# Optimization experiments

Measured on AMD Instinct MI355X. Metric: run time of the kernel, lower is better.

Reference implementation:

```python
import jax, jax.numpy as jnp
import numpy as np

D_STATE = 16
D_CONV = 4


def rmsnorm(x, w, eps=1e-6):
    # normalize over last (channel) axis
    return x * jax.lax.rsqrt(jnp.mean(x * x, axis=-1, keepdims=True) + eps) * w


def silu(x):
    return x * jax.nn.sigmoid(x)


def mamba(x, in_proj_w, conv1d_w, conv1d_b, x_proj_w, dt_proj_w, dt_proj_b, A_log, D_param, out_proj_w):
    # x: [B, L, C], d_inner == C (expand=1)
    B, L, C = x.shape
    dt_rank = dt_proj_w.shape[1]
    xz = jnp.einsum('blc,ec->ble', x, in_proj_w)  # [B, L, 2C]
    u, z = jnp.split(xz, 2, axis=-1)
    # causal depthwise conv1d over time (pad left d_conv-1)
    uc = jax.lax.conv_general_dilated(
        u.transpose(0, 2, 1), conv1d_w[:, None, :], (1,), [(D_CONV - 1, 0)],
        dimension_numbers=('NCH', 'OIH', 'NCH'), feature_group_count=C)
    u = silu((uc + conv1d_b[None, :, None]).transpose(0, 2, 1))  # [B, L, C]
    x_dbl = jnp.einsum('blc,ec->ble', u, x_proj_w)  # [B, L, dt_rank + 2*N]
    dt, Bm, Cm = jnp.split(x_dbl, [dt_rank, dt_rank + D_STATE], axis=-1)
    delta = jax.nn.softplus(jnp.einsum('blr,dr->bld', dt, dt_proj_w) + dt_proj_b)  # [B, L, C]
    A = -jnp.exp(A_log)  # [C, N]
    deltaA = jnp.exp(delta[..., None] * A)              # [B, L, C, N]
    deltaBu = (delta * u)[..., None] * Bm[:, :, None, :]  # [B, L, C, N]

    def step(h, inp):
        dA, dBu, c = inp
        h = dA * h + dBu
        return h, jnp.einsum('bdn,bn->bd', h, c)

    h0 = jnp.zeros((B, C, D_STATE), x.dtype)
    _, ys = jax.lax.scan(step, h0, (deltaA.transpose(1, 0, 2, 3),
                                    deltaBu.transpose(1, 0, 2, 3),
                                    Cm.transpose(1, 0, 2)))
    y = ys.transpose(1, 0, 2) + u * D_param  # [B, L, C]
    y = y * silu(z)
    return jnp.einsum('bld,od->blo', y, out_proj_w)


def reference(x, norm_w, in_proj_w, conv1d_w, conv1d_b, x_proj_w, dt_proj_w, dt_proj_b,
              A_log, D_param, out_proj_w, scale_mod, dw_w, dw_b, res_scale):
    B, C, H, W = x.shape
    x_cl = x.transpose(0, 2, 3, 1)              # [B, H, W, C]
    xn_cl = rmsnorm(x_cl, norm_w)
    x_norm = xn_cl.transpose(0, 3, 1, 2)        # [B, C, H, W]
    # bidirectional Mamba over flattened spatial sequence
    x_flat = xn_cl.reshape(B, H * W, C)
    mparams = (in_proj_w, conv1d_w, conv1d_b, x_proj_w, dt_proj_w, dt_proj_b, A_log, D_param, out_proj_w)
    fwd = mamba(x_flat, *mparams)
    bwd = jnp.flip(mamba(jnp.flip(x_flat, axis=1), *mparams), axis=1)
    g = (fwd + bwd) * scale_mod
    global_feat = g.reshape(B, H, W, C).transpose(0, 3, 1, 2)
    # local spatial gating: sigmoid(depthwise 3x3 conv) * x_norm
    conv = jax.lax.conv_general_dilated(
        x_norm, dw_w[:, None, :, :], (1, 1), [(1, 1), (1, 1)],
        dimension_numbers=('NCHW', 'OIHW', 'NCHW'), feature_group_count=C)
    local_feat = jax.nn.sigmoid(conv + dw_b[None, :, None, None]) * x_norm
    return x + res_scale * (global_feat + local_feat)


def setup_inputs() -> dict:
    key = jax.random.key(0)
    ks = jax.random.split(key, 10)
    B, C, H, W = 8, 384, 32, 32
    dt_rank = 24  # ceil(384 / 16)
    s = 0.02
    f32 = jnp.float32
    return {
        'x': jax.random.normal(ks[0], (B, C, H, W), f32),
        'norm_w': jnp.ones((C,), f32),
        'in_proj_w': jax.random.normal(ks[1], (2 * C, C), f32) * s,
        'conv1d_w': jax.random.normal(ks[2], (C, D_CONV), f32) * 0.2,
        'conv1d_b': jnp.zeros((C,), f32),
        'x_proj_w': jax.random.normal(ks[3], (dt_rank + 2 * D_STATE, C), f32) * s,
        'dt_proj_w': jax.random.normal(ks[4], (C, dt_rank), f32) * 0.1,
        'dt_proj_b': jax.random.uniform(ks[5], (C,), f32, -4.0, -2.0),
        'A_log': jnp.log(jnp.tile(jnp.arange(1, D_STATE + 1, dtype=f32), (C, 1))),
        'D_param': jnp.ones((C,), f32),
        'out_proj_w': jax.random.normal(ks[6], (C, C), f32) * s,
        'scale_mod': jnp.full((1,), 0.25, f32),
        'dw_w': jax.random.normal(ks[7], (C, 3, 3), f32) * 0.1,
        'dw_b': jnp.zeros((C,), f32),
        'res_scale': jnp.full((1,), 0.5, f32),
    }
```

## Files before the change

kernel.cpp:

```cpp
#include <hip/hip_runtime.h>
#include <hip/hip_bf16.h>


typedef __attribute__((ext_vector_type(8))) short bf16x8;
typedef __attribute__((ext_vector_type(8))) unsigned short u16x8;
typedef __attribute__((ext_vector_type(4))) float f32x4;

#define L2E 1.44269504088896340736f

static __device__ __forceinline__ unsigned short f2bf(float f) {
  unsigned int u = __builtin_bit_cast(unsigned int, f);
  u += 0x7fff + ((u >> 16) & 1);
  return (unsigned short)(u >> 16);
}
static __device__ __forceinline__ float bf2f(unsigned short u) {
  unsigned int v = (unsigned int)u << 16;
  return __builtin_bit_cast(float, v);
}

#define GLOAD_LDS16(g, l)                                             \
  __builtin_amdgcn_global_load_lds(                                   \
      (const __attribute__((address_space(1))) unsigned int*)(g),     \
      (__attribute__((address_space(3))) unsigned int*)(l), 16, 0, 0)

__global__ __launch_bounds__(256) void prep_k(
    const float* __restrict__ in_w, const float* __restrict__ x_w,
    const float* __restrict__ dt_w, const float* __restrict__ out_w,
    const float* __restrict__ A_log, const float* __restrict__ nw,
    unsigned short* __restrict__ W_in, unsigned short* __restrict__ W_x,
    unsigned short* __restrict__ W_dt, unsigned short* __restrict__ W_out,
    float* __restrict__ A2) {
  int idx = blockIdx.x * 256 + threadIdx.x;
  switch (blockIdx.y) {
    case 0: if (idx < 768 * 384) W_in[idx] = f2bf(in_w[idx] * nw[idx % 384]); break;
    case 1: if (idx < 64 * 384) { int n = idx / 384, k = idx - n * 384;
              W_x[idx] = f2bf(n < 56 ? x_w[n * 384 + k] : 0.f); } break;
    case 2: if (idx < 384 * 32) { int n = idx >> 5, k = idx & 31;
              W_dt[idx] = f2bf(k < 24 ? dt_w[n * 24 + k] : 0.f); } break;
    case 3: if (idx < 384 * 384) W_out[idx] = f2bf(out_w[idx]); break;
    case 4: if (idx < 384 * 16) A2[idx] = -expf(A_log[idx]) * L2E; break;
  }
}

__global__ __launch_bounds__(256) void transpose_k(
    const float* __restrict__ x, unsigned short* __restrict__ xb,
    float* __restrict__ nf) {
  const int b = blockIdx.y;
  const int l0 = blockIdx.x * 32;
  const int tid = threadIdx.x;
  const int cr = tid >> 5, lw = tid & 31;
  const int cj = tid & 63, lr = tid >> 6;
  __shared__ float t64[64][33];
  __shared__ float part[8][33];
  float acc = 0.f;
  for (int cc = 0; cc < 6; ++cc) {
    #pragma unroll
    for (int k = 0; k < 8; ++k) {
      int cp = k * 8 + cr;
      int c = cc * 64 + cp;
      float v = x[(((size_t)(b * 384 + c)) << 10) + l0 + lw];
      t64[cp][lw] = v;
      acc = fmaf(v, v, acc);
    }
    __syncthreads();
    #pragma unroll
    for (int k2 = 0; k2 < 8; ++k2) {
      int ll = lr + 4 * k2;
      xb[((size_t)((b << 10) + l0 + ll)) * 384 + cc * 64 + cj] = f2bf(t64[cj][ll]);
    }
    __syncthreads();
  }
  part[cr][lw] = acc;
  __syncthreads();
  if (tid < 32) {
    float s = part[0][tid] + part[1][tid] + part[2][tid] + part[3][tid] +
              part[4][tid] + part[5][tid] + part[6][tid] + part[7][tid];
    nf[(b << 10) + l0 + tid] = rsqrtf(s * (1.f / 384.f) + 1e-6f);
  }
}

template <int EPI, int SUMIN>
__global__ __launch_bounds__(256) void gemm128_k(
    const unsigned short* __restrict__ A0u, const unsigned short* __restrict__ A1u,
    const unsigned short* __restrict__ Bw, int K, int N,
    float* __restrict__ outf, unsigned short* __restrict__ outb,
    const float* __restrict__ aux) {
  __shared__ __attribute__((aligned(16))) unsigned short As[128 * 32];
  __shared__ __attribute__((aligned(16))) unsigned short Bs[128 * 32];
  const int n0 = blockIdx.x * 128, m0 = blockIdx.y * 128;
  const int tid = threadIdx.x;
  const int lane = tid & 63, wave = tid >> 6;
  const int wm = wave >> 1, wn = wave & 1;
  const int fr = lane & 15, ks = (lane >> 4) * 8;
  const int row = tid >> 2, colseg = (tid & 3) * 8;
  const unsigned short* pA0 = A0u + (size_t)(m0 + row) * K + colseg;
  const unsigned short* pA1 = A0u + (size_t)(m0 + 64 + row) * K + colseg;
  const unsigned short* pB0 = Bw + (size_t)(n0 + row) * K + colseg;
  const unsigned short* pB1 = Bw + (size_t)(n0 + 64 + row) * K + colseg;
  unsigned short* lA0 = As + wave * 512;
  unsigned short* lA1 = As + 2048 + wave * 512;
  unsigned short* lB0 = Bs + wave * 512;
  unsigned short* lB1 = Bs + 2048 + wave * 512;
  f32x4 acc[4][4] = {};
  for (int k0 = 0; k0 < K; k0 += 32) {
    __syncthreads();
    if (SUMIN) {
      #pragma unroll
      for (int p = 0; p < 2; ++p) {
        int r = p * 64 + row;
        u16x8 va = *(const u16x8*)&A0u[(size_t)(m0 + r) * K + k0 + colseg];
        u16x8 vb = *(const u16x8*)&A1u[(size_t)(m0 + r) * K + k0 + colseg];
        u16x8 s;
        #pragma unroll
        for (int j = 0; j < 8; ++j) s[j] = f2bf(bf2f(va[j]) + bf2f(vb[j]));
        *(u16x8*)&As[r * 32 + colseg] = s;
      }
    } else {
      GLOAD_LDS16(pA0, lA0);
      GLOAD_LDS16(pA1, lA1);
      pA0 += 32; pA1 += 32;
    }
    GLOAD_LDS16(pB0, lB0);
    GLOAD_LDS16(pB1, lB1);
    pB0 += 32; pB1 += 32;
    __syncthreads();
    bf16x8 af[4], bf[4];
    #pragma unroll
    for (int mi = 0; mi < 4; ++mi)
      af[mi] = *(const bf16x8*)&As[(wm * 64 + mi * 16 + fr) * 32 + ks];
    #pragma unroll
    for (int ni = 0; ni < 4; ++ni)
      bf[ni] = *(const bf16x8*)&Bs[(wn * 64 + ni * 16 + fr) * 32 + ks];
    #pragma unroll
    for (int mi = 0; mi < 4; ++mi)
      #pragma unroll
      for (int ni = 0; ni < 4; ++ni)
        acc[mi][ni] = __builtin_amdgcn_mfma_f32_16x16x32_bf16(af[mi], bf[ni], acc[mi][ni], 0, 0, 0);
  }
  #pragma unroll
  for (int mi = 0; mi < 4; ++mi)
    #pragma unroll
    for (int ni = 0; ni < 4; ++ni)
      #pragma unroll
      for (int j = 0; j < 4; ++j) {
        int m = m0 + wm * 64 + mi * 16 + (lane >> 4) * 4 + j;
        int n = n0 + wn * 64 + ni * 16 + fr;
        float v = acc[mi][ni][j];
        if (EPI == 0) {
          outb[(size_t)m * N + n] = f2bf(v * aux[m]);
        } else {
          outf[(size_t)m * N + n] = v * aux[0];
        }
      }
}

template <int EPI>
__global__ __launch_bounds__(256) void gemm_k(
    const unsigned short* __restrict__ A0u, const unsigned short* __restrict__ A1u,
    const unsigned short* __restrict__ Bw, int K, int N,
    float* __restrict__ of0, float* __restrict__ of1,
    unsigned short* __restrict__ ob0, unsigned short* __restrict__ ob1,
    const float* __restrict__ aux) {
  const unsigned short* A = blockIdx.z ? A1u : A0u;
  float* outf = blockIdx.z ? of1 : of0;
  unsigned short* outb = blockIdx.z ? ob1 : ob0;
  __shared__ unsigned short As[64][40];
  __shared__ unsigned short Bs[64][40];
  const int n0 = blockIdx.x * 64, m0 = blockIdx.y * 64;
  const int tid = threadIdx.x;
  const int lane = tid & 63, wave = tid >> 6;
  const int wm = wave >> 1, wn = wave & 1;
  const int lrow = tid >> 2, lseg = (tid & 3) * 8;
  const int fr = lane & 15, ks = (lane >> 4) * 8;
  f32x4 acc[2][2] = {};
  for (int k0 = 0; k0 < K; k0 += 32) {
    __syncthreads();
    *(bf16x8*)&As[lrow][lseg] = *(const bf16x8*)&A[(size_t)(m0 + lrow) * K + k0 + lseg];
    *(bf16x8*)&Bs[lrow][lseg] = *(const bf16x8*)&Bw[(size_t)(n0 + lrow) * K + k0 + lseg];
    __syncthreads();
    bf16x8 a0 = *(const bf16x8*)&As[wm * 32 + fr][ks];
    bf16x8 a1 = *(const bf16x8*)&As[wm * 32 + 16 + fr][ks];
    bf16x8 b0 = *(const bf16x8*)&Bs[wn * 32 + fr][ks];
    bf16x8 b1 = *(const bf16x8*)&Bs[wn * 32 + 16 + fr][ks];
    acc[0][0] = __builtin_amdgcn_mfma_f32_16x16x32_bf16(a0, b0, acc[0][0], 0, 0, 0);
    acc[0][1] = __builtin_amdgcn_mfma_f32_16x16x32_bf16(a0, b1, acc[0][1], 0, 0, 0);
    acc[1][0] = __builtin_amdgcn_mfma_f32_16x16x32_bf16(a1, b0, acc[1][0], 0, 0, 0);
    acc[1][1] = __builtin_amdgcn_mfma_f32_16x16x32_bf16(a1, b1, acc[1][1], 0, 0, 0);
  }
  #pragma unroll
  for (int mi = 0; mi < 2; ++mi)
    #pragma unroll
    for (int ni = 0; ni < 2; ++ni)
      #pragma unroll
      for (int j = 0; j < 4; ++j) {
        int m = m0 + wm * 32 + mi * 16 + (lane >> 4) * 4 + j;
        int n = n0 + wn * 32 + ni * 16 + (lane & 15);
        float v = acc[mi][ni][j];
        if (EPI == 1) {
          if (n < 24) outb[m * 32 + n] = f2bf(v);
          else if (n < 32) outb[m * 32 + n] = 0;
          if (n >= 24 && n < 56) outf[m * 32 + (n - 24)] = v;
        } else {
          float t = v + aux[n];
          float sp = (t > 20.f) ? t : log1pf(expf(t));
          outb[(size_t)m * N + n] = f2bf(sp);
        }
      }
}

__global__ __launch_bounds__(384) void conv_silu_k(
    const unsigned short* __restrict__ xz, const float* __restrict__ cw,
    const float* __restrict__ cb,
    unsigned short* __restrict__ ub0, unsigned short* __restrict__ ub1) {
  const int st = blockIdx.x, b = blockIdx.y, dir = blockIdx.z;
  const int c = threadIdx.x;
  const int s0 = st * 8;
  const float w0 = cw[c * 4 + 0], w1 = cw[c * 4 + 1];
  const float w2 = cw[c * 4 + 2], w3 = cw[c * 4 + 3];
  const float bb = cb[c];
  unsigned short* ub = dir ? ub1 : ub0;
  float xv[11];
  #pragma unroll
  for (int k = 0; k < 11; ++k) {
    int j = s0 - 3 + k;
    float v = 0.f;
    if (j >= 0) {
      int t = dir ? (1023 - j) : j;
      v = bf2f(xz[(size_t)((b << 10) + t) * 768 + c]);
    }
    xv[k] = v;
  }
  #pragma unroll
  for (int s = 0; s < 8; ++s) {
    float a = bb + xv[s] * w0 + xv[s + 1] * w1 + xv[s + 2] * w2 + xv[s + 3] * w3;
    float uv = a * __builtin_amdgcn_rcpf(1.f + __builtin_amdgcn_exp2f(-a * L2E));
    ub[(size_t)((b << 10) + s0 + s) * 384 + c] = f2bf(uv);
  }
}

__global__ __launch_bounds__(512) void scan1_k(
    const unsigned short* __restrict__ de0, const unsigned short* __restrict__ de1,
    const unsigned short* __restrict__ ub0, const unsigned short* __restrict__ ub1,
    const float* __restrict__ bc0, const float* __restrict__ bc1,
    const float* __restrict__ A2, float* __restrict__ PH) {
  const int ct = blockIdx.x, b = blockIdx.y;
  const int dir = blockIdx.z >> 4, seg = blockIdx.z & 15;
  const unsigned short* del = dir ? de1 : de0;
  const unsigned short* uu  = dir ? ub1 : ub0;
  const float* bc  = dir ? bc1 : bc0;
  const int tid = threadIdx.x;
  const int lane = tid & 63, wave = tid >> 6;
  const int n = lane & 15, cg = lane >> 4;
  const int cl = wave * 4 + cg;
  const int c = ct * 32 + cl;
  const float a2 = A2[c * 16 + n];
  const size_t base = ((size_t)b << 10) + seg * 64;
  __shared__ __attribute__((aligned(16))) float sd[32][68];
  __shared__ __attribute__((aligned(16))) float su[32][68];
  __shared__ __attribute__((aligned(16))) float sB[16][68];
  const int li = tid >> 5, lj = tid & 31;
  const int li3 = tid >> 4, lj3 = tid & 15;
  unsigned short rd[4], ru[4];
  float rb[2];
  #pragma unroll
  for (int k = 0; k < 4; ++k) {
    size_t rowi = base + k * 16 + li;
    rd[k] = del[rowi * 384 + ct * 32 + lj];
    ru[k] = uu [rowi * 384 + ct * 32 + lj];
  }
  #pragma unroll
  for (int k = 0; k < 2; ++k)
    rb[k] = bc[(base + k * 32 + li3) * 32 + lj3];
  #pragma unroll
  for (int k = 0; k < 4; ++k) {
    sd[lj][k * 16 + li] = bf2f(rd[k]);
    su[lj][k * 16 + li] = bf2f(ru[k]);
  }
  #pragma unroll
  for (int k = 0; k < 2; ++k) sB[lj3][k * 32 + li3] = rb[k];
  __syncthreads();
  float h = 0.f, P = 1.f;
  for (int ch = 0; ch < 4; ++ch) {
    f32x4 dv[4], uv4[4], bmv[4];
    #pragma unroll
    for (int r = 0; r < 4; ++r) {
      dv[r]  = *(const f32x4*)&sd[cl][ch * 16 + r * 4];
      uv4[r] = *(const f32x4*)&su[cl][ch * 16 + r * 4];
      bmv[r] = *(const f32x4*)&sB[n][ch * 16 + r * 4];
    }
    #pragma unroll
    for (int i = 0; i < 16; ++i) {
      float dd = dv[i >> 2][i & 3];
      float dA = __builtin_amdgcn_exp2f(dd * a2);
      h = fmaf(dA, h, dd * uv4[i >> 2][i & 3] * bmv[i >> 2][i & 3]);
      P *= dA;
    }
  }
  size_t o = (size_t)((dir * 8 + b) * 16 + seg) * 6144 + c * 16 + n;
  *(float2*)&PH[o * 2] = make_float2(P, h);
}

__global__ __launch_bounds__(512) void scan2_k(
    const unsigned short* __restrict__ de0, const unsigned short* __restrict__ de1,
    const unsigned short* __restrict__ ub0, const unsigned short* __restrict__ ub1,
    const float* __restrict__ bc0, const float* __restrict__ bc1,
    const unsigned short* __restrict__ xz, const float* __restrict__ A2,
    const float* __restrict__ Dp, const float* __restrict__ PH,
    unsigned short* __restrict__ Sb0, unsigned short* __restrict__ Sb1) {
  const int ct = blockIdx.x, b = blockIdx.y;
  const int dir = blockIdx.z >> 4, seg = blockIdx.z & 15;
  const unsigned short* del = dir ? de1 : de0;
  const unsigned short* uu  = dir ? ub1 : ub0;
  const float* bc  = dir ? bc1 : bc0;
  unsigned short* S = dir ? Sb1 : Sb0;
  const int tid = threadIdx.x;
  const int lane = tid & 63, wave = tid >> 6;
  const int n = lane & 15, cg = lane >> 4;
  const int cl = wave * 4 + cg;
  const int c = ct * 32 + cl;
  const float a2 = A2[c * 16 + n];
  const float dpc = Dp[c];
  const size_t base = (size_t)b << 10;
  const int segoff = seg * 64;
  __shared__ __attribute__((aligned(16))) float sd[32][68];
  __shared__ __attribute__((aligned(16))) float su[32][68];
  __shared__ __attribute__((aligned(16))) float sz[32][68];
  __shared__ __attribute__((aligned(16))) float sbc[32][68];
  const int li = tid >> 5, lj = tid & 31;
  unsigned short rd[4], ru[4], rz[4];
  float rb[4];
  #pragma unroll
  for (int k = 0; k < 4; ++k) {
    size_t rowi = base + segoff + k * 16 + li;
    rd[k] = del[rowi * 384 + ct * 32 + lj];
    ru[k] = uu [rowi * 384 + ct * 32 + lj];
    int t = dir ? (1023 - (segoff + k * 16 + li)) : (segoff + k * 16 + li);
    rz[k] = xz[(base + t) * 768 + 384 + ct * 32 + lj];
    rb[k] = bc[rowi * 32 + lj];
  }
  float h = 0.f;
  {
    size_t rb2 = ((size_t)((dir * 8 + b) * 16) * 6144 + c * 16 + n) * 2;
    #pragma unroll
    for (int s = 0; s < 15; ++s) {
      float2 ph = *(const float2*)&PH[rb2 + (size_t)s * 12288];
      h = (s < seg) ? fmaf(ph.x, h, ph.y) : h;
    }
  }
  #pragma unroll
  for (int k = 0; k < 4; ++k) {
    sd[lj][k * 16 + li] = bf2f(rd[k]);
    su[lj][k * 16 + li] = bf2f(ru[k]);
    sz[lj][k * 16 + li] = bf2f(rz[k]);
    sbc[lj][k * 16 + li] = rb[k];
  }
  __syncthreads();
  for (int ch = 0; ch < 4; ++ch) {
    f32x4 dv[4], uv4[4], bmv[4], cmv[4];
    #pragma unroll
    for (int r = 0; r < 4; ++r) {
      dv[r]  = *(const f32x4*)&sd[cl][ch * 16 + r * 4];
      uv4[r] = *(const f32x4*)&su[cl][ch * 16 + r * 4];
      bmv[r] = *(const f32x4*)&sbc[n][ch * 16 + r * 4];
      cmv[r] = *(const f32x4*)&sbc[16 + n][ch * 16 + r * 4];
    }
    float p[16];
    #pragma unroll
    for (int i = 0; i < 16; ++i) {
      float dd = dv[i >> 2][i & 3];
      float dA = __builtin_amdgcn_exp2f(dd * a2);
      h = fmaf(dA, h, dd * uv4[i >> 2][i & 3] * bmv[i >> 2][i & 3]);
      p[i] = h * cmv[i >> 2][i & 3];
    }
    float q8[8];
    #pragma unroll
    for (int j = 0; j < 8; ++j) {
      float send = (n & 8) ? p[j] : p[j + 8];
      float recv = __shfl_xor(send, 8);
      float keep = (n & 8) ? p[j + 8] : p[j];
      q8[j] = keep + recv;
    }
    float q4[4];
    #pragma unroll
    for (int j = 0; j < 4; ++j) {
      float send = (n & 4) ? q8[j] : q8[j + 4];
      float recv = __shfl_xor(send, 4);
      float keep = (n & 4) ? q8[j + 4] : q8[j];
      q4[j] = keep + recv;
    }
    float q2[2];
    #pragma unroll
    for (int j = 0; j < 2; ++j) {
      float send = (n & 2) ? q4[j] : q4[j + 2];
      float recv = __shfl_xor(send, 2);
      float keep = (n & 2) ? q4[j + 2] : q4[j];
      q2[j] = keep + recv;
    }
    float send = (n & 1) ? q2[0] : q2[1];
    float recv = __shfl_xor(send, 1);
    float keep = (n & 1) ? q2[1] : q2[0];
    float ysum = keep + recv;
    float uvn = su[cl][ch * 16 + n];
    float zz  = sz[cl][ch * 16 + n];
    float sig = __builtin_amdgcn_rcpf(1.f + __builtin_amdgcn_exp2f(-zz * L2E));
    float y = (ysum + uvn * dpc) * (zz * sig);
    int s = segoff + ch * 16 + n;
    int t = dir ? (1023 - s) : s;
    S[(base + t) * 384 + c] = f2bf(y);
  }
}

__global__ __launch_bounds__(256) void final_k(
    const float* __restrict__ G, const unsigned short* __restrict__ xb,
    const float* __restrict__ nf, const float* __restrict__ nw,
    const float* __restrict__ x, const float* __restrict__ dww,
    const float* __restrict__ dwb, const float* __restrict__ rs,
    float* __restrict__ out) {
  __shared__ float tile[64][33];
  __shared__ float wq[9][64];
  __shared__ float bbs[64], nws[64];
  const int l0 = blockIdx.x * 32, c0 = blockIdx.y * 64, b = blockIdx.z;
  const int tid = threadIdx.x;
  for (int i = tid; i < 576; i += 256) {
    int c = i / 9, q = i - c * 9;
    wq[q][c] = dww[(size_t)(c0 + c) * 9 + q] * nw[c0 + c];
  }
  if (tid < 64) { bbs[tid] = dwb[c0 + tid]; nws[tid] = nw[c0 + tid]; }
  __syncthreads();
  {
    const int oct = tid & 7, li = tid >> 3;
    const int l = l0 + li;
    const int hh = l >> 5, ww = l & 31;
    float acc[8];
    {
      f32x4 ba = *(const f32x4*)&bbs[oct * 8];
      f32x4 bb2 = *(const f32x4*)&bbs[oct * 8 + 4];
      #pragma unroll
      for (int j = 0; j < 4; ++j) { acc[j] = ba[j]; acc[j + 4] = bb2[j]; }
    }
    #pragma unroll
    for (int di = -1; di <= 1; ++di) {
      int h2 = hh + di;
      if (h2 < 0 || h2 > 31) continue;
      #pragma unroll
      for (int dj = -1; dj <= 1; ++dj) {
        int w2 = ww + dj;
        if (w2 < 0 || w2 > 31) continue;
        int lp = h2 * 32 + w2;
        float nfl = nf[(b << 10) + lp];
        u16x8 v = *(const u16x8*)&xb[(size_t)((b << 10) + lp) * 384 + c0 + oct * 8];
        int q = (di + 1) * 3 + (dj + 1);
        f32x4 wa = *(const f32x4*)&wq[q][oct * 8];
        f32x4 wb = *(const f32x4*)&wq[q][oct * 8 + 4];
        #pragma unroll
        for (int j = 0; j < 4; ++j) {
          acc[j]     = fmaf(bf2f(v[j]) * nfl, wa[j], acc[j]);
          acc[j + 4] = fmaf(bf2f(v[j + 4]) * nfl, wb[j], acc[j + 4]);
        }
      }
    }
    size_t ri = (size_t)((b << 10) + l) * 384 + c0 + oct * 8;
    float nfl0 = nf[(b << 10) + l];
    u16x8 xc = *(const u16x8*)&xb[ri];
    f32x4 g0 = *(const f32x4*)&G[ri];
    f32x4 g1 = *(const f32x4*)&G[ri + 4];
    #pragma unroll
    for (int j = 0; j < 8; ++j) {
      float xv = bf2f(xc[j]) * nfl0 * nws[oct * 8 + j];
      float sig = __builtin_amdgcn_rcpf(1.f + __builtin_amdgcn_exp2f(-acc[j] * L2E));
      float gg = (j < 4) ? g0[j] : g1[j - 4];
      tile[oct * 8 + j][li] = gg + xv * sig;
    }
  }
  __syncthreads();
  {
    const int lw = tid & 31, cr = tid >> 5;
    const float rsv = rs[0];
    for (int p = 0; p < 8; ++p) {
      int c = c0 + p * 8 + cr;
      size_t o = ((size_t)(b * 384 + c) << 10) + l0 + lw;
      out[o] = x[o] + rsv * tile[p * 8 + cr][lw];
    }
  }
}

extern "C" void kernel_launch(void* const* d_in, const int* in_sizes, int n_in,
                              void* d_out, int out_size, void* d_ws, size_t ws_size,
                              hipStream_t stream) {
  const float* x         = (const float*)d_in[0];
  const float* norm_w    = (const float*)d_in[1];
  const float* in_proj_w = (const float*)d_in[2];
  const float* conv1d_w  = (const float*)d_in[3];
  const float* conv1d_b  = (const float*)d_in[4];
  const float* x_proj_w  = (const float*)d_in[5];
  const float* dt_proj_w = (const float*)d_in[6];
  const float* dt_proj_b = (const float*)d_in[7];
  const float* A_log     = (const float*)d_in[8];
  const float* D_param   = (const float*)d_in[9];
  const float* out_proj_w= (const float*)d_in[10];
  const float* scale_mod = (const float*)d_in[11];
  const float* dw_w      = (const float*)d_in[12];
  const float* dw_b      = (const float*)d_in[13];
  const float* res_scale = (const float*)d_in[14];
  float* out = (float*)d_out;

  char* base = (char*)d_ws;
  size_t off = 0;
  auto alloc = [&](size_t bytes) {
    off = (off + 255) & ~(size_t)255;
    void* p = base + off;
    off += bytes;
    return p;
  };
  const size_t B_BLC = (size_t)8192 * 384 * 2;

  unsigned short* xb   = (unsigned short*)alloc(B_BLC);
  float*          nf   = (float*)alloc((size_t)8192 * 4);
  unsigned short* xz   = (unsigned short*)alloc((size_t)8192 * 768 * 2);
  unsigned short* u_b0 = (unsigned short*)alloc(B_BLC);
  unsigned short* u_b1 = (unsigned short*)alloc(B_BLC);
  unsigned short* dtp0 = (unsigned short*)alloc((size_t)8192 * 32 * 2);
  unsigned short* dtp1 = (unsigned short*)alloc((size_t)8192 * 32 * 2);
  float*          bc0  = (float*)alloc((size_t)8192 * 32 * 4);
  float*          bc1  = (float*)alloc((size_t)8192 * 32 * 4);
  unsigned short* de0  = (unsigned short*)alloc(B_BLC);
  unsigned short* de1  = (unsigned short*)alloc(B_BLC);
  unsigned short* Sb0  = (unsigned short*)alloc(B_BLC);
  unsigned short* Sb1  = (unsigned short*)alloc(B_BLC);
  float*          PH   = (float*)alloc((size_t)1572864 * 2 * 4);
  unsigned short* W_in = (unsigned short*)alloc((size_t)768 * 384 * 2);
  unsigned short* W_x  = (unsigned short*)alloc((size_t)64 * 384 * 2);
  unsigned short* W_dt = (unsigned short*)alloc((size_t)384 * 32 * 2);
  unsigned short* W_out= (unsigned short*)alloc((size_t)384 * 384 * 2);
  float*          A2   = (float*)alloc((size_t)384 * 16 * 4);
  float*          G    = (float*)alloc((size_t)8192 * 384 * 4);

  prep_k<<<dim3(1152, 5), 256, 0, stream>>>(in_proj_w, x_proj_w, dt_proj_w,
                                            out_proj_w, A_log, norm_w,
                                            W_in, W_x, W_dt, W_out, A2);
  transpose_k<<<dim3(32, 8), 256, 0, stream>>>(x, xb, nf);
  gemm128_k<0, 0><<<dim3(6, 64), 256, 0, stream>>>(xb, xb, W_in, 384, 768,
                                                   nullptr, xz, nf);
  conv_silu_k<<<dim3(128, 8, 2), 384, 0, stream>>>(xz, conv1d_w, conv1d_b,
                                                   u_b0, u_b1);
  gemm_k<1><<<dim3(1, 128, 2), 256, 0, stream>>>(u_b0, u_b1, W_x, 384, 64,
                                                 bc0, bc1, dtp0, dtp1, nullptr);
  gemm_k<2><<<dim3(6, 128, 2), 256, 0, stream>>>(dtp0, dtp1, W_dt, 32, 384,
                                                 nullptr, nullptr, de0, de1,
                                                 dt_proj_b);
  scan1_k<<<dim3(12, 8, 32), 512, 0, stream>>>(de0, de1, u_b0, u_b1, bc0, bc1,
                                               A2, PH);
  scan2_k<<<dim3(12, 8, 32), 512, 0, stream>>>(de0, de1, u_b0, u_b1, bc0, bc1,
                                               xz, A2, D_param, PH, Sb0, Sb1);
  gemm128_k<3, 1><<<dim3(3, 64), 256, 0, stream>>>(Sb0, Sb1, W_out, 384, 384,
                                                   G, nullptr, scale_mod);
  final_k<<<dim3(32, 6, 8), 256, 0, stream>>>(G, xb, nf, norm_w, x, dw_w, dw_b,
                                              res_scale, out);
}
```

Baseline: 247.3 us.

## Fold dt_proj into x_proj weights, store out-proj result in bf16, stage scan output

Precomputes a combined weight dt_proj_w·x_proj_w[:24], so delta and the B/C projections come from one 128-tiled GEMM with a softplus epilogue. This replaces two small GEMM launches and the dt intermediate buffer. The out-proj GEMM now writes bf16 instead of fp32 to halve that intermediate's traffic, at some precision cost. scan1 precomputes delta*u when staging, and scan2 stages its outputs in LDS so global stores are coalesced. The combined GEMM does more arithmetic (K=384 over N=512 instead of rank 24).

```diff
diff --git a/kernel.cpp b/kernel.cpp
--- a/kernel.cpp
+++ b/kernel.cpp
@@ -27,18 +27,24 @@
     const float* __restrict__ in_w, const float* __restrict__ x_w,
     const float* __restrict__ dt_w, const float* __restrict__ out_w,
     const float* __restrict__ A_log, const float* __restrict__ nw,
-    unsigned short* __restrict__ W_in, unsigned short* __restrict__ W_x,
-    unsigned short* __restrict__ W_dt, unsigned short* __restrict__ W_out,
-    float* __restrict__ A2) {
+    unsigned short* __restrict__ W_in, unsigned short* __restrict__ W_out,
+    unsigned short* __restrict__ Wcomb, float* __restrict__ A2) {
   int idx = blockIdx.x * 256 + threadIdx.x;
   switch (blockIdx.y) {
     case 0: if (idx < 768 * 384) W_in[idx] = f2bf(in_w[idx] * nw[idx % 384]); break;
-    case 1: if (idx < 64 * 384) { int n = idx / 384, k = idx - n * 384;
-              W_x[idx] = f2bf(n < 56 ? x_w[n * 384 + k] : 0.f); } break;
-    case 2: if (idx < 384 * 32) { int n = idx >> 5, k = idx & 31;
-              W_dt[idx] = f2bf(k < 24 ? dt_w[n * 24 + k] : 0.f); } break;
-    case 3: if (idx < 384 * 384) W_out[idx] = f2bf(out_w[idx]); break;
-    case 4: if (idx < 384 * 16) A2[idx] = -expf(A_log[idx]) * L2E; break;
+    case 1: if (idx < 384 * 384) W_out[idx] = f2bf(out_w[idx]); break;
+    case 2: if (idx < 384 * 16) A2[idx] = -expf(A_log[idx]) * L2E; break;
+    case 3: if (idx < 384 * 384) {
+        int o = idx / 384, c = idx - o * 384;
+        float s = 0.f;
+        #pragma unroll
+        for (int r = 0; r < 24; ++r) s += dt_w[o * 24 + r] * x_w[r * 384 + c];
+        Wcomb[idx] = f2bf(s);
+      } break;
+    case 4: if (idx < 128 * 384) {
+        int n = idx / 384, k = idx - n * 384;
+        Wcomb[147456 + idx] = f2bf(n < 32 ? x_w[(24 + n) * 384 + k] : 0.f);
+      } break;
   }
 }
 
@@ -83,8 +89,12 @@
 __global__ __launch_bounds__(256) void gemm128_k(
     const unsigned short* __restrict__ A0u, const unsigned short* __restrict__ A1u,
     const unsigned short* __restrict__ Bw, int K, int N,
-    float* __restrict__ outf, unsigned short* __restrict__ outb,
+    unsigned short* __restrict__ ob0, unsigned short* __restrict__ ob1,
+    float* __restrict__ of0, float* __restrict__ of1,
     const float* __restrict__ aux) {
+  const unsigned short* Au = (EPI == 2 && blockIdx.z) ? A1u : A0u;
+  unsigned short* ob = (EPI == 2 && blockIdx.z) ? ob1 : ob0;
+  float* of = (EPI == 2 && blockIdx.z) ? of1 : of0;
   __shared__ __attribute__((aligned(16))) unsigned short As[128 * 32];
   __shared__ __attribute__((aligned(16))) unsigned short Bs[128 * 32];
   const int n0 = blockIdx.x * 128, m0 = blockIdx.y * 128;
@@ -93,8 +103,8 @@
   const int wm = wave >> 1, wn = wave & 1;
   const int fr = lane & 15, ks = (lane >> 4) * 8;
   const int row = tid >> 2, colseg = (tid & 3) * 8;
-  const unsigned short* pA0 = A0u + (size_t)(m0 + row) * K + colseg;
-  const unsigned short* pA1 = A0u + (size_t)(m0 + 64 + row) * K + colseg;
+  const unsigned short* pA0 = Au + (size_t)(m0 + row) * K + colseg;
+  const unsigned short* pA1 = Au + (size_t)(m0 + 64 + row) * K + colseg;
   const unsigned short* pB0 = Bw + (size_t)(n0 + row) * K + colseg;
   const unsigned short* pB1 = Bw + (size_t)(n0 + 64 + row) * K + colseg;
   unsigned short* lA0 = As + wave * 512;
@@ -124,18 +134,18 @@
     GLOAD_LDS16(pB1, lB1);
     pB0 += 32; pB1 += 32;
     __syncthreads();
-    bf16x8 af[4], bf[4];
+    bf16x8 af[4], bfr[4];
     #pragma unroll
     for (int mi = 0; mi < 4; ++mi)
       af[mi] = *(const bf16x8*)&As[(wm * 64 + mi * 16 + fr) * 32 + ks];
     #pragma unroll
     for (int ni = 0; ni < 4; ++ni)
-      bf[ni] = *(const bf16x8*)&Bs[(wn * 64 + ni * 16 + fr) * 32 + ks];
+      bfr[ni] = *(const bf16x8*)&Bs[(wn * 64 + ni * 16 + fr) * 32 + ks];
     #pragma unroll
     for (int mi = 0; mi < 4; ++mi)
       #pragma unroll
       for (int ni = 0; ni < 4; ++ni)
-        acc[mi][ni] = __builtin_amdgcn_mfma_f32_16x16x32_bf16(af[mi], bf[ni], acc[mi][ni], 0, 0, 0);
+        acc[mi][ni] = __builtin_amdgcn_mfma_f32_16x16x32_bf16(af[mi], bfr[ni], acc[mi][ni], 0, 0, 0);
   }
   #pragma unroll
   for (int mi = 0; mi < 4; ++mi)
@@ -147,63 +157,17 @@
         int n = n0 + wn * 64 + ni * 16 + fr;
         float v = acc[mi][ni][j];
         if (EPI == 0) {
-          outb[(size_t)m * N + n] = f2bf(v * aux[m]);
+          ob0[(size_t)m * N + n] = f2bf(v * aux[m]);
+        } else if (EPI == 2) {
+          if (n < 384) {
+            float t = v + aux[n];
+            float sp = (t > 20.f) ? t : log1pf(expf(t));
+            ob[(size_t)m * 384 + n] = f2bf(sp);
+          } else if (n < 416) {
+            of[(size_t)m * 32 + (n - 384)] = v;
+          }
         } else {
-          outf[(size_t)m * N + n] = v * aux[0];
-        }
-      }
-}
-
-template <int EPI>
-__global__ __launch_bounds__(256) void gemm_k(
-    const unsigned short* __restrict__ A0u, const unsigned short* __restrict__ A1u,
-    const unsigned short* __restrict__ Bw, int K, int N,
-    float* __restrict__ of0, float* __restrict__ of1,
-    unsigned short* __restrict__ ob0, unsigned short* __restrict__ ob1,
-    const float* __restrict__ aux) {
-  const unsigned short* A = blockIdx.z ? A1u : A0u;
-  float* outf = blockIdx.z ? of1 : of0;
-  unsigned short* outb = blockIdx.z ? ob1 : ob0;
-  __shared__ unsigned short As[64][40];
-  __shared__ unsigned short Bs[64][40];
-  const int n0 = blockIdx.x * 64, m0 = blockIdx.y * 64;
-  const int tid = threadIdx.x;
-  const int lane = tid & 63, wave = tid >> 6;
-  const int wm = wave >> 1, wn = wave & 1;
-  const int lrow = tid >> 2, lseg = (tid & 3) * 8;
-  const int fr = lane & 15, ks = (lane >> 4) * 8;
-  f32x4 acc[2][2] = {};
-  for (int k0 = 0; k0 < K; k0 += 32) {
-    __syncthreads();
-    *(bf16x8*)&As[lrow][lseg] = *(const bf16x8*)&A[(size_t)(m0 + lrow) * K + k0 + lseg];
-    *(bf16x8*)&Bs[lrow][lseg] = *(const bf16x8*)&Bw[(size_t)(n0 + lrow) * K + k0 + lseg];
-    __syncthreads();
-    bf16x8 a0 = *(const bf16x8*)&As[wm * 32 + fr][ks];
-    bf16x8 a1 = *(const bf16x8*)&As[wm * 32 + 16 + fr][ks];
-    bf16x8 b0 = *(const bf16x8*)&Bs[wn * 32 + fr][ks];
-    bf16x8 b1 = *(const bf16x8*)&Bs[wn * 32 + 16 + fr][ks];
-    acc[0][0] = __builtin_amdgcn_mfma_f32_16x16x32_bf16(a0, b0, acc[0][0], 0, 0, 0);
-    acc[0][1] = __builtin_amdgcn_mfma_f32_16x16x32_bf16(a0, b1, acc[0][1], 0, 0, 0);
-    acc[1][0] = __builtin_amdgcn_mfma_f32_16x16x32_bf16(a1, b0, acc[1][0], 0, 0, 0);
-    acc[1][1] = __builtin_amdgcn_mfma_f32_16x16x32_bf16(a1, b1, acc[1][1], 0, 0, 0);
-  }
-  #pragma unroll
-  for (int mi = 0; mi < 2; ++mi)
-    #pragma unroll
-    for (int ni = 0; ni < 2; ++ni)
-      #pragma unroll
-      for (int j = 0; j < 4; ++j) {
-        int m = m0 + wm * 32 + mi * 16 + (lane >> 4) * 4 + j;
-        int n = n0 + wn * 32 + ni * 16 + (lane & 15);
-        float v = acc[mi][ni][j];
-        if (EPI == 1) {
-          if (n < 24) outb[m * 32 + n] = f2bf(v);
-          else if (n < 32) outb[m * 32 + n] = 0;
-          if (n >= 24 && n < 56) outf[m * 32 + (n - 24)] = v;
-        } else {
-          float t = v + aux[n];
-          float sp = (t > 20.f) ? t : log1pf(expf(t));
-          outb[(size_t)m * N + n] = f2bf(sp);
+          ob0[(size_t)m * N + n] = f2bf(v * aux[0]);
         }
       }
 }
@@ -273,26 +237,26 @@
     rb[k] = bc[(base + k * 32 + li3) * 32 + lj3];
   #pragma unroll
   for (int k = 0; k < 4; ++k) {
-    sd[lj][k * 16 + li] = bf2f(rd[k]);
-    su[lj][k * 16 + li] = bf2f(ru[k]);
+    float dd = bf2f(rd[k]);
+    sd[lj][k * 16 + li] = dd;
+    su[lj][k * 16 + li] = dd * bf2f(ru[k]);
   }
   #pragma unroll
   for (int k = 0; k < 2; ++k) sB[lj3][k * 32 + li3] = rb[k];
   __syncthreads();
   float h = 0.f, P = 1.f;
   for (int ch = 0; ch < 4; ++ch) {
-    f32x4 dv[4], uv4[4], bmv[4];
+    f32x4 dv[4], duv[4], bmv[4];
     #pragma unroll
     for (int r = 0; r < 4; ++r) {
       dv[r]  = *(const f32x4*)&sd[cl][ch * 16 + r * 4];
-      uv4[r] = *(const f32x4*)&su[cl][ch * 16 + r * 4];
+      duv[r] = *(const f32x4*)&su[cl][ch * 16 + r * 4];
       bmv[r] = *(const f32x4*)&sB[n][ch * 16 + r * 4];
     }
     #pragma unroll
     for (int i = 0; i < 16; ++i) {
-      float dd = dv[i >> 2][i & 3];
-      float dA = __builtin_amdgcn_exp2f(dd * a2);
-      h = fmaf(dA, h, dd * uv4[i >> 2][i & 3] * bmv[i >> 2][i & 3]);
+      float dA = __builtin_amdgcn_exp2f(dv[i >> 2][i & 3] * a2);
+      h = fmaf(dA, h, duv[i >> 2][i & 3] * bmv[i >> 2][i & 3]);
       P *= dA;
     }
   }
@@ -320,27 +284,28 @@
   const int c = ct * 32 + cl;
   const float a2 = A2[c * 16 + n];
   const float dpc = Dp[c];
-  const size_t base = (size_t)b << 10;
+  const size_t bb_ = (size_t)b << 10;
   const int segoff = seg * 64;
   __shared__ __attribute__((aligned(16))) float sd[32][68];
   __shared__ __attribute__((aligned(16))) float su[32][68];
   __shared__ __attribute__((aligned(16))) float sz[32][68];
   __shared__ __attribute__((aligned(16))) float sbc[32][68];
+  __shared__ __attribute__((aligned(16))) unsigned short sy[64 * 36];
   const int li = tid >> 5, lj = tid & 31;
   unsigned short rd[4], ru[4], rz[4];
   float rb[4];
   #pragma unroll
   for (int k = 0; k < 4; ++k) {
-    size_t rowi = base + segoff + k * 16 + li;
+    size_t rowi = bb_ + segoff + k * 16 + li;
     rd[k] = del[rowi * 384 + ct * 32 + lj];
     ru[k] = uu [rowi * 384 + ct * 32 + lj];
-    int t = dir ? (1023 - (segoff + k * 16 + li)) : (segoff + k * 16 + li);
-    rz[k] = xz[(base + t) * 768 + 384 + ct * 32 + lj];
+    int tz = dir ? (1023 - (segoff + k * 16 + li)) : (segoff + k * 16 + li);
+    rz[k] = xz[(bb_ + tz) * 768 + 384 + ct * 32 + lj];
     rb[k] = bc[rowi * 32 + lj];
   }
   float h = 0.f;
   {
-    size_t rb2 = ((size_t)((dir * 8 + b) * 16) * 6144 + c * 16 + n) * 2;
+    size_t rb2 = (((size_t)(dir * 8 + b) * 16) * 6144 + c * 16 + n) * 2;
     #pragma unroll
     for (int s = 0; s < 15; ++s) {
       float2 ph = *(const float2*)&PH[rb2 + (size_t)s * 12288];
@@ -404,14 +369,20 @@
     float zz  = sz[cl][ch * 16 + n];
     float sig = __builtin_amdgcn_rcpf(1.f + __builtin_amdgcn_exp2f(-zz * L2E));
     float y = (ysum + uvn * dpc) * (zz * sig);
-    int s = segoff + ch * 16 + n;
-    int t = dir ? (1023 - s) : s;
-    S[(base + t) * 384 + c] = f2bf(y);
+    sy[(ch * 16 + n) * 36 + cl] = f2bf(y);
+  }
+  __syncthreads();
+  {
+    const int t = tid >> 3, cq = (tid & 7) * 4;
+    int tg = segoff + t;
+    int trow = dir ? (1023 - tg) : tg;
+    *(ushort4*)&S[(bb_ + trow) * 384 + ct * 32 + cq] =
+        *(const ushort4*)&sy[t * 36 + cq];
   }
 }
 
 __global__ __launch_bounds__(256) void final_k(
-    const float* __restrict__ G, const unsigned short* __restrict__ xb,
+    const unsigned short* __restrict__ Gb, const unsigned short* __restrict__ xb,
     const float* __restrict__ nf, const float* __restrict__ nw,
     const float* __restrict__ x, const float* __restrict__ dww,
     const float* __restrict__ dwb, const float* __restrict__ rs,
@@ -462,14 +433,12 @@
     size_t ri = (size_t)((b << 10) + l) * 384 + c0 + oct * 8;
     float nfl0 = nf[(b << 10) + l];
     u16x8 xc = *(const u16x8*)&xb[ri];
-    f32x4 g0 = *(const f32x4*)&G[ri];
-    f32x4 g1 = *(const f32x4*)&G[ri + 4];
+    u16x8 gv = *(const u16x8*)&Gb[ri];
     #pragma unroll
     for (int j = 0; j < 8; ++j) {
       float xv = bf2f(xc[j]) * nfl0 * nws[oct * 8 + j];
       float sig = __builtin_amdgcn_rcpf(1.f + __builtin_amdgcn_exp2f(-acc[j] * L2E));
-      float gg = (j < 4) ? g0[j] : g1[j - 4];
-      tile[oct * 8 + j][li] = gg + xv * sig;
+      tile[oct * 8 + j][li] = bf2f(gv[j]) + xv * sig;
     }
   }
   __syncthreads();
@@ -519,8 +488,6 @@
   unsigned short* xz   = (unsigned short*)alloc((size_t)8192 * 768 * 2);
   unsigned short* u_b0 = (unsigned short*)alloc(B_BLC);
   unsigned short* u_b1 = (unsigned short*)alloc(B_BLC);
-  unsigned short* dtp0 = (unsigned short*)alloc((size_t)8192 * 32 * 2);
-  unsigned short* dtp1 = (unsigned short*)alloc((size_t)8192 * 32 * 2);
   float*          bc0  = (float*)alloc((size_t)8192 * 32 * 4);
   float*          bc1  = (float*)alloc((size_t)8192 * 32 * 4);
   unsigned short* de0  = (unsigned short*)alloc(B_BLC);
@@ -529,31 +496,29 @@
   unsigned short* Sb1  = (unsigned short*)alloc(B_BLC);
   float*          PH   = (float*)alloc((size_t)1572864 * 2 * 4);
   unsigned short* W_in = (unsigned short*)alloc((size_t)768 * 384 * 2);
-  unsigned short* W_x  = (unsigned short*)alloc((size_t)64 * 384 * 2);
-  unsigned short* W_dt = (unsigned short*)alloc((size_t)384 * 32 * 2);
   unsigned short* W_out= (unsigned short*)alloc((size_t)384 * 384 * 2);
+  unsigned short* Wcomb= (unsigned short*)alloc((size_t)512 * 384 * 2);
   float*          A2   = (float*)alloc((size_t)384 * 16 * 4);
-  float*          G    = (float*)alloc((size_t)8192 * 384 * 4);
+  unsigned short* Gb   = (unsigned short*)alloc(B_BLC);
 
   prep_k<<<dim3(1152, 5), 256, 0, stream>>>(in_proj_w, x_proj_w, dt_proj_w,
                                             out_proj_w, A_log, norm_w,
-                                            W_in, W_x, W_dt, W_out, A2);
+                                            W_in, W_out, Wcomb, A2);
   transpose_k<<<dim3(32, 8), 256, 0, stream>>>(x, xb, nf);
   gemm128_k<0, 0><<<dim3(6, 64), 256, 0, stream>>>(xb, xb, W_in, 384, 768,
-                                                   nullptr, xz, nf);
+                                                   xz, xz, nullptr, nullptr, nf);
   conv_silu_k<<<dim3(128, 8, 2), 384, 0, stream>>>(xz, conv1d_w, conv1d_b,
                                                    u_b0, u_b1);
-  gemm_k<1><<<dim3(1, 128, 2), 256, 0, stream>>>(u_b0, u_b1, W_x, 384, 64,
-                                                 bc0, bc1, dtp0, dtp1, nullptr);
-  gemm_k<2><<<dim3(6, 128, 2), 256, 0, stream>>>(dtp0, dtp1, W_dt, 32, 384,
-                                                 nullptr, nullptr, de0, de1,
-                                                 dt_proj_b);
+  gemm128_k<2, 0><<<dim3(4, 64, 2), 256, 0, stream>>>(u_b0, u_b1, Wcomb, 384, 512,
+                                                      de0, de1, bc0, bc1,
+                                                      dt_proj_b);
   scan1_k<<<dim3(12, 8, 32), 512, 0, stream>>>(de0, de1, u_b0, u_b1, bc0, bc1,
                                                A2, PH);
   scan2_k<<<dim3(12, 8, 32), 512, 0, stream>>>(de0, de1, u_b0, u_b1, bc0, bc1,
                                                xz, A2, D_param, PH, Sb0, Sb1);
   gemm128_k<3, 1><<<dim3(3, 64), 256, 0, stream>>>(Sb0, Sb1, W_out, 384, 384,
-                                                   G, nullptr, scale_mod);
-  final_k<<<dim3(32, 6, 8), 256, 0, stream>>>(G, xb, nf, norm_w, x, dw_w, dw_b,
+                                                   Gb, Gb, nullptr, nullptr,
+                                                   scale_mod);
+  final_k<<<dim3(32, 6, 8), 256, 0, stream>>>(Gb, xb, nf, norm_w, x, dw_w, dw_b,
                                               res_scale, out);
 }
```

Result: slower. 263.4 us (+6.5%).
